# Kernel tuning notes

Measured on AMD Instinct MI355X. Metric: run time of the kernel, lower is better.

Reference implementation:

```python
import jax, jax.numpy as jnp
import numpy as np

B, L, C, H = 4, 1024, 768, 12
D = C // H  # head_ch = 64


def setup_inputs() -> dict:
    key = jax.random.key(0)
    ks = jax.random.split(key, 8)
    s = 1.0 / np.sqrt(C)
    return {
        "inputs_q": jax.random.normal(ks[0], (B, L, C), jnp.float32),
        "inputs_kv": jax.random.normal(ks[1], (B, L, C), jnp.float32),
        "Wq": jax.random.normal(ks[2], (C, H * D), jnp.float32) * s,
        "Wk": jax.random.normal(ks[3], (C, H * D), jnp.float32) * s,
        "Wv": jax.random.normal(ks[4], (C, H * D), jnp.float32) * s,
        "Wout": jax.random.normal(ks[5], (H * D, C), jnp.float32) * s,
        "W_pre": jax.random.normal(ks[6], (H, H), jnp.float32) * (1.0 / np.sqrt(H)),
        "W_post": jax.random.normal(ks[7], (H, H), jnp.float32) * (1.0 / np.sqrt(H)),
    }


def reference(inputs_q, inputs_kv, Wq, Wk, Wv, Wout, W_pre, W_post):
    # Linear projections (no bias), split into heads: b l (h d) -> b h l d
    def split_heads(x):
        b, l, _ = x.shape
        return x.reshape(b, l, H, D).transpose(0, 2, 1, 3)

    q = split_heads(inputs_q @ Wq) / jnp.sqrt(jnp.asarray(D, inputs_q.dtype))
    k = split_heads(inputs_kv @ Wk)
    v = split_heads(inputs_kv @ Wv)

    # Attention logits [b, h, l, k]
    weights = jnp.einsum('bhld,bhkd->bhlk', q, k)
    # Talking-heads: learned cross-head mixing pre-softmax
    weights = jnp.einsum('bhlk,hi->bilk', weights, W_pre)
    weights = jax.nn.softmax(weights, axis=-1)
    # Talking-heads post-softmax mixing
    weights = jnp.einsum('bhlk,hi->bilk', weights, W_post)

    scores = jnp.einsum('bhlk,bhkd->bhld', weights, v)
    scores = scores.transpose(0, 2, 1, 3).reshape(B, L, H * D)  # b l (h d)
    return scores @ Wout
```

## Files before the change

### kernel.cpp

```cpp
#include <hip/hip_runtime.h>
#include <hip/hip_bf16.h>

#define BB 4
#define LL 1024
#define CC 768
#define HH 12
#define DD 64

typedef unsigned short ushort_t;
typedef __attribute__((ext_vector_type(8))) short bf16x8;
typedef __attribute__((ext_vector_type(4))) float f32x4;
typedef __attribute__((ext_vector_type(2))) float f32x2;
typedef __attribute__((ext_vector_type(2))) unsigned u32x2;

__device__ inline ushort_t f2bf(float x) {
    union { float f; unsigned u; } v; v.f = x;
    unsigned r = (v.u + 0x7FFFu + ((v.u >> 16) & 1u)) >> 16;
    return (ushort_t)r;
}
__device__ inline float u2f(unsigned u) {
    union { unsigned u; float f; } v; v.u = u;
    return v.f;
}
__device__ inline unsigned pack2bf(float lo, float hi) {
    union { __hip_bfloat162 v; unsigned u; } r;
    r.v = __float22bfloat162_rn(make_float2(lo, hi));
    return r.u;
}

__device__ inline void stage_rows(const ushort_t* __restrict__ g, int stride,
                                  ushort_t* lds, int nbytes, int wave, int lane) {
    const int ko = (lane & 3) << 3;
    const int rsub = lane >> 2;
    for (int off = wave * 1024; off < nbytes; off += 4096) {
        int row = (off >> 6) + rsub;
        __builtin_amdgcn_global_load_lds(
            (const __attribute__((address_space(1))) void*)(g + (size_t)row * stride + ko),
            (__attribute__((address_space(3))) void*)(lds + (off >> 1)),
            16, 0, 0);
    }
}

__global__ __launch_bounds__(256) void prep(const float* __restrict__ q, const float* __restrict__ kv,
                                            const float* __restrict__ w0, const float* __restrict__ w1,
                                            const float* __restrict__ w2, const float* __restrict__ w3,
                                            ushort_t* __restrict__ qo, ushort_t* __restrict__ kvo,
                                            ushort_t* __restrict__ o0, ushort_t* __restrict__ o1,
                                            ushort_t* __restrict__ o2, ushort_t* __restrict__ o3,
                                            float* __restrict__ Zp) {
    __shared__ float t[32][33];
    const int bx = blockIdx.x;
    if (bx < 3072) {
        const float* src = bx < 1536 ? q : kv;
        ushort_t* dst = bx < 1536 ? qo : kvo;
        int bb = bx < 1536 ? bx : bx - 1536;
        size_t i = ((size_t)bb * 256 + threadIdx.x) * 8;
        float4 a = *(const float4*)(src + i);
        float4 b = *(const float4*)(src + i + 4);
        ushort_t u[8] = {f2bf(a.x), f2bf(a.y), f2bf(a.z), f2bf(a.w),
                         f2bf(b.x), f2bf(b.y), f2bf(b.z), f2bf(b.w)};
        *(uint4*)(dst + i) = *(uint4*)u;
    } else if (bx < 5376) {
        int w = bx - 3072;
        int z = w / 576, rem = w % 576;
        const float* W = z == 0 ? w0 : z == 1 ? w1 : z == 2 ? w2 : w3;
        ushort_t* Wt   = z == 0 ? o0 : z == 1 ? o1 : z == 2 ? o2 : o3;
        const int c = threadIdx.x & 31, r0 = threadIdx.x >> 5;
        const int kb = (rem / 24) * 32, nb = (rem % 24) * 32;
#pragma unroll
        for (int i = 0; i < 4; ++i)
            t[r0 + 8 * i][c] = W[(size_t)(kb + r0 + 8 * i) * CC + nb + c];
        __syncthreads();
#pragma unroll
        for (int i = 0; i < 4; ++i)
            Wt[(size_t)(nb + r0 + 8 * i) * CC + kb + c] = f2bf(t[c][r0 + 8 * i]);
    } else {
        Zp[(bx - 5376) * 256 + threadIdx.x] = 0.f;
    }
}

__global__ __launch_bounds__(256) void proj_gemm(const ushort_t* __restrict__ Aq,
                                                 const ushort_t* __restrict__ Akv,
                                                 const ushort_t* __restrict__ Wqt,
                                                 const ushort_t* __restrict__ Wkt,
                                                 const ushort_t* __restrict__ Wvt,
                                                 ushort_t* __restrict__ Qo,
                                                 ushort_t* __restrict__ Ko,
                                                 ushort_t* __restrict__ Vto) {
    const int z = blockIdx.z;
    const ushort_t* A  = (z == 0) ? Aq : Akv;
    const ushort_t* Wt = (z == 0) ? Wqt : (z == 1 ? Wkt : Wvt);

    __shared__ __align__(16) ushort_t a_lds[128 * 32];
    __shared__ __align__(16) ushort_t b_lds[128 * 32];

    const int tid = threadIdx.x;
    const int bm = blockIdx.x * 128, bn = blockIdx.y * 128;
    const int wave = tid >> 6, lane = tid & 63;
    const int quad = lane >> 4, lq = lane & 15;
    const int wr = wave >> 1, wc = wave & 1;

    f32x4 acc[4][4] = {};

    for (int k0 = 0; k0 < CC; k0 += 32) {
        stage_rows(A + (size_t)bm * CC + k0, CC, a_lds, 8192, wave, lane);
        stage_rows(Wt + (size_t)bn * CC + k0, CC, b_lds, 8192, wave, lane);
        __syncthreads();
        bf16x8 af[4], bfr[4];
#pragma unroll
        for (int mi = 0; mi < 4; ++mi)
            af[mi] = *(bf16x8*)&a_lds[(wr * 64 + mi * 16 + lq) * 32 + quad * 8];
#pragma unroll
        for (int ni = 0; ni < 4; ++ni)
            bfr[ni] = *(bf16x8*)&b_lds[(wc * 64 + ni * 16 + lq) * 32 + quad * 8];
#pragma unroll
        for (int mi = 0; mi < 4; ++mi)
#pragma unroll
            for (int ni = 0; ni < 4; ++ni)
                acc[mi][ni] = __builtin_amdgcn_mfma_f32_16x16x32_bf16(af[mi], bfr[ni], acc[mi][ni], 0, 0, 0);
        __syncthreads();
    }

    const float scale = (z == 0) ? 0.125f : 1.0f;
#pragma unroll
    for (int mi = 0; mi < 4; ++mi)
#pragma unroll
        for (int ni = 0; ni < 4; ++ni)
#pragma unroll
            for (int r = 0; r < 4; ++r) {
                int row = bm + wr * 64 + mi * 16 + quad * 4 + r;
                int col = bn + wc * 64 + ni * 16 + lq;
                int b = row >> 10, l = row & 1023, h = col >> 6, d = col & 63;
                ushort_t v = f2bf(acc[mi][ni][r] * scale);
                if (z == 2) {
                    Vto[((size_t)(b * HH + h) * DD + d) * LL + l] = v;
                } else {
                    size_t off = (size_t)(b * HH + h) * (LL * DD)
                               + (size_t)(((l >> 4) * 8 + (d >> 3)) * 128 + (l & 15) * 8 + (d & 7));
                    if (z == 0) Qo[off] = v;
                    else        Ko[off] = v;
                }
            }
}

__global__ __launch_bounds__(256) void qk_premix(const ushort_t* __restrict__ Qf,
                                                 const ushort_t* __restrict__ Kf,
                                                 const float* __restrict__ Wpre,
                                                 ushort_t* __restrict__ E,
                                                 float* __restrict__ Z) {
    const int tid = threadIdx.x;
    const int lane = tid & 63, wave = tid >> 6;
    const int quad = lane >> 4, lq = lane & 15;
    const int wr = wave >> 1, wc = wave & 1;

    const int x = blockIdx.x;
    const int xcd = x & 7;
    const int b = xcd >> 1;
    const int s = x >> 3;
    const int bk = (s & 31) << 5;
    const int bl = ((((s >> 5) << 1) | (xcd & 1))) << 5;

    const ushort_t* Kp = Kf + (size_t)b * HH * LL * DD
                       + (size_t)(((bk >> 4) + wr) * 1024 + quad * 128 + lq * 8);
    const ushort_t* Qp = Qf + (size_t)b * HH * LL * DD
                       + (size_t)(((bl >> 4) + wc) * 1024 + quad * 128 + lq * 8);

    f32x4 acc[HH] = {};
#pragma unroll
    for (int h = 0; h < HH; ++h) {
        const size_t ho = (size_t)h * (LL * DD);
        bf16x8 ka0 = *(const bf16x8*)(Kp + ho);
        bf16x8 ka1 = *(const bf16x8*)(Kp + ho + 512);
        bf16x8 qb0 = *(const bf16x8*)(Qp + ho);
        bf16x8 qb1 = *(const bf16x8*)(Qp + ho + 512);
        acc[h] = __builtin_amdgcn_mfma_f32_16x16x32_bf16(ka0, qb0, acc[h], 0, 0, 0);
        acc[h] = __builtin_amdgcn_mfma_f32_16x16x32_bf16(ka1, qb1, acc[h], 0, 0, 0);
    }

    unsigned pk[6][4];
#pragma unroll
    for (int i2 = 0; i2 < 6; ++i2) {
        f32x4 m0 = {}, m1 = {};
#pragma unroll
        for (int h = 0; h < HH; ++h) {
            m0 += acc[h] * Wpre[h * HH + 2 * i2];
            m1 += acc[h] * Wpre[h * HH + 2 * i2 + 1];
        }
#pragma unroll
        for (int r = 0; r < 4; ++r)
            pk[i2][r] = pack2bf(__expf(m0[r]), __expf(m1[r]));
    }

    float zp[HH];
#pragma unroll
    for (int i2 = 0; i2 < 6; ++i2) {
        float s0 = 0.f, s1 = 0.f;
#pragma unroll
        for (int r = 0; r < 4; ++r) {
            s0 += u2f(pk[i2][r] << 16);
            s1 += u2f(pk[i2][r] & 0xFFFF0000u);
        }
        zp[2 * i2] = s0; zp[2 * i2 + 1] = s1;
    }
#pragma unroll
    for (int i = 0; i < HH; ++i) {
        zp[i] += __shfl_xor(zp[i], 16);
        zp[i] += __shfl_xor(zp[i], 32);
    }
    if (quad == 0) {
#pragma unroll
        for (int i = 0; i < HH; ++i)
            atomicAdd(&Z[((size_t)b * HH + i) * LL + bl + wc * 16 + lq], zp[i]);
    }

    const int ltw = (bl >> 4) + wc;
#pragma unroll
    for (int r = 0; r < 4; ++r) {
        const int k = bk + wr * 16 + quad * 4 + r;
        ushort_t* ep = E + (((size_t)(b * 64 + ltw) * 1024 + k) * 16 + lq) * 12;
        u32x2 s0; s0.x = pk[0][r]; s0.y = pk[1][r];
        u32x2 s1; s1.x = pk[2][r]; s1.y = pk[3][r];
        u32x2 s2; s2.x = pk[4][r]; s2.y = pk[5][r];
        __builtin_nontemporal_store(s0, (u32x2*)ep);
        __builtin_nontemporal_store(s1, (u32x2*)(ep + 4));
        __builtin_nontemporal_store(s2, (u32x2*)(ep + 8));
    }
}

__global__ __launch_bounds__(256, 1) void pv_postmix(const ushort_t* __restrict__ E,
                                                     const ushort_t* __restrict__ Vt,
                                                     const float* __restrict__ Wpost,
                                                     const float* __restrict__ Z,
                                                     ushort_t* __restrict__ att) {
    const int tid = threadIdx.x;
    const int lane = tid & 63, wave = tid >> 6;
    const int quad = lane >> 4, lq = lane & 15;
    const int hh0 = wave * 3;

    const int bid = blockIdx.x;
    const int xcd = bid & 7;
    const int b = xcd >> 1;
    const int lt = ((bid >> 3) << 1) | (xcd & 1);
    const int bl = lt << 4;

    float wp[HH][3];
#pragma unroll
    for (int h = 0; h < HH; ++h)
#pragma unroll
        for (int ii = 0; ii < 3; ++ii)
            wp[h][ii] = Wpost[h * HH + hh0 + ii];

    float invZ[HH];
#pragma unroll
    for (int h = 0; h < HH; ++h)
        invZ[h] = 1.0f / Z[((size_t)b * HH + h) * LL + bl + lq];

    const ushort_t* eslice = E + (size_t)(b * 64 + lt) * (1024 * 192)
                           + (size_t)(quad * 8) * 192 + lq * 12;
    const ushort_t* vbase = Vt + ((size_t)(b * HH + hh0) * DD + lq) * LL + quad * 8;

    f32x4 acc[3][4] = {};
    u32x2 eA[24], eB[24];
    bf16x8 vf[12];

#define LOADE(dst, kt_, k0_)                                                              \
    do {                                                                                  \
        const ushort_t* ep_ = eslice + (size_t)((kt_) * 64 + (k0_) * 32) * 192;           \
        _Pragma("unroll")                                                                 \
        for (int j_ = 0; j_ < 8; ++j_)                                                    \
            _Pragma("unroll")                                                             \
            for (int c_ = 0; c_ < 3; ++c_)                                                \
                dst[j_ * 3 + c_] = *(const u32x2*)(ep_ + j_ * 192 + c_ * 4);              \
    } while (0)

#define LOADV(kt_, k0_)                                                                   \
    do {                                                                                  \
        _Pragma("unroll")                                                                 \
        for (int ii_ = 0; ii_ < 3; ++ii_)                                                 \
            _Pragma("unroll")                                                             \
            for (int dq_ = 0; dq_ < 4; ++dq_)                                             \
                vf[ii_ * 4 + dq_] = *(const bf16x8*)(vbase                                \
                    + (size_t)(ii_ * DD + dq_ * 16) * LL + (kt_) * 64 + (k0_) * 32);      \
    } while (0)

#define HALF(src)                                                                         \
    do {                                                                                  \
        union { bf16x8 v; unsigned d[4]; } pa_[3];                                        \
        _Pragma("unroll")                                                                 \
        for (int j2_ = 0; j2_ < 4; ++j2_) {                                               \
            float p0_[3] = {0.f, 0.f, 0.f}, p1_[3] = {0.f, 0.f, 0.f};                     \
            _Pragma("unroll")                                                             \
            for (int c_ = 0; c_ < 3; ++c_) {                                              \
                u32x2 ea_ = src[(2 * j2_) * 3 + c_];                                      \
                u32x2 eb_ = src[(2 * j2_ + 1) * 3 + c_];                                  \
                float f0_ = u2f(ea_.x << 16)         * invZ[4 * c_ + 0];                  \
                float f1_ = u2f(ea_.x & 0xFFFF0000u) * invZ[4 * c_ + 1];                  \
                float f2_ = u2f(ea_.y << 16)         * invZ[4 * c_ + 2];                  \
                float f3_ = u2f(ea_.y & 0xFFFF0000u) * invZ[4 * c_ + 3];                  \
                float g0_ = u2f(eb_.x << 16)         * invZ[4 * c_ + 0];                  \
                float g1_ = u2f(eb_.x & 0xFFFF0000u) * invZ[4 * c_ + 1];                  \
                float g2_ = u2f(eb_.y << 16)         * invZ[4 * c_ + 2];                  \
                float g3_ = u2f(eb_.y & 0xFFFF0000u) * invZ[4 * c_ + 3];                  \
                _Pragma("unroll")                                                         \
                for (int ii_ = 0; ii_ < 3; ++ii_) {                                       \
                    p0_[ii_] += f0_ * wp[4 * c_ + 0][ii_] + f1_ * wp[4 * c_ + 1][ii_]     \
                              + f2_ * wp[4 * c_ + 2][ii_] + f3_ * wp[4 * c_ + 3][ii_];    \
                    p1_[ii_] += g0_ * wp[4 * c_ + 0][ii_] + g1_ * wp[4 * c_ + 1][ii_]     \
                              + g2_ * wp[4 * c_ + 2][ii_] + g3_ * wp[4 * c_ + 3][ii_];    \
                }                                                                         \
            }                                                                             \
            _Pragma("unroll")                                                             \
            for (int ii_ = 0; ii_ < 3; ++ii_)                                             \
                pa_[ii_].d[j2_] = pack2bf(p0_[ii_], p1_[ii_]);                            \
        }                                                                                 \
        _Pragma("unroll")                                                                 \
        for (int ii_ = 0; ii_ < 3; ++ii_)                                                 \
            _Pragma("unroll")                                                             \
            for (int dq_ = 0; dq_ < 4; ++dq_)                                             \
                acc[ii_][dq_] = __builtin_amdgcn_mfma_f32_16x16x32_bf16(                  \
                    pa_[ii_].v, vf[ii_ * 4 + dq_], acc[ii_][dq_], 0, 0, 0);               \
    } while (0)

    LOADE(eA, 0, 0);
#pragma unroll 1
    for (int kt = 0; kt < 16; ++kt) {
        LOADE(eB, kt, 1);
        LOADV(kt, 0);
        HALF(eA);
        if (kt < 15) LOADE(eA, kt + 1, 0);
        LOADV(kt, 1);
        HALF(eB);
    }
#undef LOADE
#undef LOADV
#undef HALF

#pragma unroll
    for (int ii = 0; ii < 3; ++ii)
#pragma unroll
        for (int dq = 0; dq < 4; ++dq)
#pragma unroll
            for (int r = 0; r < 4; ++r)
                att[((size_t)b * LL + bl + quad * 4 + r) * CC + (hh0 + ii) * 64 + dq * 16 + lq] =
                    f2bf(acc[ii][dq][r]);
}

__global__ __launch_bounds__(256) void out_gemm(const ushort_t* __restrict__ A,
                                                const ushort_t* __restrict__ Wt,
                                                float* __restrict__ out) {
    __shared__ __align__(16) ushort_t a_lds[128 * 32];
    __shared__ __align__(16) ushort_t b_lds[64 * 32];

    const int tid = threadIdx.x;
    const int bm = blockIdx.x * 128, bn = blockIdx.y * 64;
    const int wave = tid >> 6, lane = tid & 63;
    const int quad = lane >> 4, lq = lane & 15;
    const int wr = wave >> 1, wc = wave & 1;

    f32x4 acc[4][2] = {};

    for (int k0 = 0; k0 < CC; k0 += 32) {
        stage_rows(A + (size_t)bm * CC + k0, CC, a_lds, 8192, wave, lane);
        stage_rows(Wt + (size_t)bn * CC + k0, CC, b_lds, 4096, wave, lane);
        __syncthreads();
        bf16x8 af[4], bfr[2];
#pragma unroll
        for (int mi = 0; mi < 4; ++mi)
            af[mi] = *(bf16x8*)&a_lds[(wr * 64 + mi * 16 + lq) * 32 + quad * 8];
#pragma unroll
        for (int ni = 0; ni < 2; ++ni)
            bfr[ni] = *(bf16x8*)&b_lds[(wc * 32 + ni * 16 + lq) * 32 + quad * 8];
#pragma unroll
        for (int mi = 0; mi < 4; ++mi)
#pragma unroll
            for (int ni = 0; ni < 2; ++ni)
                acc[mi][ni] = __builtin_amdgcn_mfma_f32_16x16x32_bf16(af[mi], bfr[ni], acc[mi][ni], 0, 0, 0);
        __syncthreads();
    }

#pragma unroll
    for (int mi = 0; mi < 4; ++mi)
#pragma unroll
        for (int ni = 0; ni < 2; ++ni)
#pragma unroll
            for (int r = 0; r < 4; ++r) {
                int row = bm + wr * 64 + mi * 16 + quad * 4 + r;
                int col = bn + wc * 32 + ni * 16 + lq;
                out[(size_t)row * CC + col] = acc[mi][ni][r];
            }
}

extern "C" void kernel_launch(void* const* d_in, const int* in_sizes, int n_in,
                              void* d_out, int out_size, void* d_ws, size_t ws_size,
                              hipStream_t stream) {
    const float* inputs_q  = (const float*)d_in[0];
    const float* inputs_kv = (const float*)d_in[1];
    const float* Wq   = (const float*)d_in[2];
    const float* Wk   = (const float*)d_in[3];
    const float* Wv   = (const float*)d_in[4];
    const float* Wout = (const float*)d_in[5];
    const float* Wpre  = (const float*)d_in[6];
    const float* Wpost = (const float*)d_in[7];
    float* out = (float*)d_out;

    const size_t nS   = (size_t)BB * HH * LL * LL;
    const size_t nQKV = (size_t)BB * HH * LL * DD;
    const size_t nW   = (size_t)CC * CC;

    ushort_t* Eb   = (ushort_t*)d_ws;
    ushort_t* Qb   = Eb + nS;
    ushort_t* Kb   = Qb + nQKV;
    ushort_t* Vtb  = Kb + nQKV;
    ushort_t* attb = Vtb + nQKV;
    ushort_t* inq  = attb + nQKV;
    ushort_t* inkv = inq + nQKV;
    ushort_t* Wqt  = inkv + nQKV;
    ushort_t* Wkt  = Wqt + nW;
    ushort_t* Wvt  = Wkt + nW;
    ushort_t* Wot  = Wvt + nW;
    float*    Zb   = (float*)(Wot + nW);

    dim3 blk(256);

    prep<<<dim3(5568), blk, 0, stream>>>(inputs_q, inputs_kv, Wq, Wk, Wv, Wout,
                                         inq, inkv, Wqt, Wkt, Wvt, Wot, Zb);
    proj_gemm<<<dim3(32, 6, 3), blk, 0, stream>>>(inq, inkv, Wqt, Wkt, Wvt, Qb, Kb, Vtb);
    qk_premix<<<dim3(4096), blk, 0, stream>>>(Qb, Kb, Wpre, Eb, Zb);
    pv_postmix<<<dim3(256), blk, 0, stream>>>(Eb, Vtb, Wpost, Zb, attb);
    out_gemm<<<dim3(32, 12), blk, 0, stream>>>(attb, Wot, out);
}
```

Measured before the change: 267.2 us.

## Split pv_postmix key range across waves with LDS reduction, 4x more blocks

pv_postmix now launches 1024 blocks instead of 256. Each block handles one group of three output heads, and its four waves split the key tiles round-robin instead of each wave owning three heads over all keys. The partial accumulators are reduced through shared memory before the bf16 store. This raises occupancy and parallelism on the 256-CU GPU, at the cost of recomputing the post-mix for every head group, which reloads E four times. The post-mix arithmetic is also rewritten with packed f32x2 operations so it can use packed FMA.

Result: no change. 271.9 us (+1.8%).

```diff
diff --git a/kernel.cpp b/kernel.cpp
--- a/kernel.cpp
+++ b/kernel.cpp
@@ -227,20 +227,24 @@
     }
 }
 
-__global__ __launch_bounds__(256, 1) void pv_postmix(const ushort_t* __restrict__ E,
+__global__ __launch_bounds__(256, 2) void pv_postmix(const ushort_t* __restrict__ E,
                                                      const ushort_t* __restrict__ Vt,
                                                      const float* __restrict__ Wpost,
                                                      const float* __restrict__ Z,
                                                      ushort_t* __restrict__ att) {
+    __shared__ __align__(16) f32x4 red[4][3][4][64];
+
     const int tid = threadIdx.x;
     const int lane = tid & 63, wave = tid >> 6;
     const int quad = lane >> 4, lq = lane & 15;
-    const int hh0 = wave * 3;
 
     const int bid = blockIdx.x;
     const int xcd = bid & 7;
     const int b = xcd >> 1;
-    const int lt = ((bid >> 3) << 1) | (xcd & 1);
+    const int s = bid >> 3;
+    const int hg = s >> 5;
+    const int hh0 = hg * 3;
+    const int lt = ((s & 31) << 1) | (xcd & 1);
     const int bl = lt << 4;
 
     float wp[HH][3];
@@ -288,30 +292,31 @@
         union { bf16x8 v; unsigned d[4]; } pa_[3];                                        \
         _Pragma("unroll")                                                                 \
         for (int j2_ = 0; j2_ < 4; ++j2_) {                                               \
-            float p0_[3] = {0.f, 0.f, 0.f}, p1_[3] = {0.f, 0.f, 0.f};                     \
+            f32x2 m_[3] = {};                                                             \
             _Pragma("unroll")                                                             \
             for (int c_ = 0; c_ < 3; ++c_) {                                              \
                 u32x2 ea_ = src[(2 * j2_) * 3 + c_];                                      \
                 u32x2 eb_ = src[(2 * j2_ + 1) * 3 + c_];                                  \
-                float f0_ = u2f(ea_.x << 16)         * invZ[4 * c_ + 0];                  \
-                float f1_ = u2f(ea_.x & 0xFFFF0000u) * invZ[4 * c_ + 1];                  \
-                float f2_ = u2f(ea_.y << 16)         * invZ[4 * c_ + 2];                  \
-                float f3_ = u2f(ea_.y & 0xFFFF0000u) * invZ[4 * c_ + 3];                  \
-                float g0_ = u2f(eb_.x << 16)         * invZ[4 * c_ + 0];                  \
-                float g1_ = u2f(eb_.x & 0xFFFF0000u) * invZ[4 * c_ + 1];                  \
-                float g2_ = u2f(eb_.y << 16)         * invZ[4 * c_ + 2];                  \
-                float g3_ = u2f(eb_.y & 0xFFFF0000u) * invZ[4 * c_ + 3];                  \
+                f32x2 h0_, h1_, h2_, h3_;                                                 \
+                h0_.x = u2f(ea_.x << 16);         h0_.y = u2f(eb_.x << 16);               \
+                h1_.x = u2f(ea_.x & 0xFFFF0000u); h1_.y = u2f(eb_.x & 0xFFFF0000u);       \
+                h2_.x = u2f(ea_.y << 16);         h2_.y = u2f(eb_.y << 16);               \
+                h3_.x = u2f(ea_.y & 0xFFFF0000u); h3_.y = u2f(eb_.y & 0xFFFF0000u);       \
+                h0_ *= invZ[4 * c_ + 0];                                                  \
+                h1_ *= invZ[4 * c_ + 1];                                                  \
+                h2_ *= invZ[4 * c_ + 2];                                                  \
+                h3_ *= invZ[4 * c_ + 3];                                                  \
                 _Pragma("unroll")                                                         \
                 for (int ii_ = 0; ii_ < 3; ++ii_) {                                       \
-                    p0_[ii_] += f0_ * wp[4 * c_ + 0][ii_] + f1_ * wp[4 * c_ + 1][ii_]     \
-                              + f2_ * wp[4 * c_ + 2][ii_] + f3_ * wp[4 * c_ + 3][ii_];    \
-                    p1_[ii_] += g0_ * wp[4 * c_ + 0][ii_] + g1_ * wp[4 * c_ + 1][ii_]     \
-                              + g2_ * wp[4 * c_ + 2][ii_] + g3_ * wp[4 * c_ + 3][ii_];    \
+                    m_[ii_] += h0_ * wp[4 * c_ + 0][ii_];                                 \
+                    m_[ii_] += h1_ * wp[4 * c_ + 1][ii_];                                 \
+                    m_[ii_] += h2_ * wp[4 * c_ + 2][ii_];                                 \
+                    m_[ii_] += h3_ * wp[4 * c_ + 3][ii_];                                 \
                 }                                                                         \
             }                                                                             \
             _Pragma("unroll")                                                             \
             for (int ii_ = 0; ii_ < 3; ++ii_)                                             \
-                pa_[ii_].d[j2_] = pack2bf(p0_[ii_], p1_[ii_]);                            \
+                pa_[ii_].d[j2_] = pack2bf(m_[ii_].x, m_[ii_].y);                          \
         }                                                                                 \
         _Pragma("unroll")                                                                 \
         for (int ii_ = 0; ii_ < 3; ++ii_)                                                 \
@@ -321,13 +326,14 @@
                     pa_[ii_].v, vf[ii_ * 4 + dq_], acc[ii_][dq_], 0, 0, 0);               \
     } while (0)
 
-    LOADE(eA, 0, 0);
+    LOADE(eA, wave, 0);
 #pragma unroll 1
-    for (int kt = 0; kt < 16; ++kt) {
+    for (int t = 0; t < 4; ++t) {
+        const int kt = wave + 4 * t;
         LOADE(eB, kt, 1);
         LOADV(kt, 0);
         HALF(eA);
-        if (kt < 15) LOADE(eA, kt + 1, 0);
+        if (t < 3) LOADE(eA, kt + 4, 0);
         LOADV(kt, 1);
         HALF(eB);
     }
@@ -339,10 +345,18 @@
     for (int ii = 0; ii < 3; ++ii)
 #pragma unroll
         for (int dq = 0; dq < 4; ++dq)
-#pragma unroll
-            for (int r = 0; r < 4; ++r)
-                att[((size_t)b * LL + bl + quad * 4 + r) * CC + (hh0 + ii) * 64 + dq * 16 + lq] =
-                    f2bf(acc[ii][dq][r]);
+            red[wave][ii][dq][lane] = acc[ii][dq];
+    __syncthreads();
+
+#pragma unroll
+    for (int ii = 0; ii < 3; ++ii) {
+        f32x4 sum = (red[0][ii][wave][lane] + red[1][ii][wave][lane])
+                  + (red[2][ii][wave][lane] + red[3][ii][wave][lane]);
+#pragma unroll
+        for (int r = 0; r < 4; ++r)
+            att[((size_t)b * LL + bl + quad * 4 + r) * CC + (hh0 + ii) * 64 + wave * 16 + lq] =
+                f2bf(sum[r]);
+    }
 }
 
 __global__ __launch_bounds__(256) void out_gemm(const ushort_t* __restrict__ A,
@@ -426,6 +440,6 @@
                                          inq, inkv, Wqt, Wkt, Wvt, Wot, Zb);
     proj_gemm<<<dim3(32, 6, 3), blk, 0, stream>>>(inq, inkv, Wqt, Wkt, Wvt, Qb, Kb, Vtb);
     qk_premix<<<dim3(4096), blk, 0, stream>>>(Qb, Kb, Wpre, Eb, Zb);
-    pv_postmix<<<dim3(256), blk, 0, stream>>>(Eb, Vtb, Wpost, Zb, attb);
+    pv_postmix<<<dim3(1024), blk, 0, stream>>>(Eb, Vtb, Wpost, Zb, attb);
     out_gemm<<<dim3(32, 12), blk, 0, stream>>>(attb, Wot, out);
 }
```
